# Kernel optimization log

Hardware: AMD Instinct MI355X
Metric: run time of the kernel (lower is better)

Reference implementation:

```python
import jax, jax.numpy as jnp
import numpy as np

B, T, D, H = 4096, 200, 128, 16
NEG = -4294967295.0  # -2**32 + 1, as in the TF source


def setup_inputs() -> dict:
    key = jax.random.key(0)
    k1, k2, k3, k4, k5 = jax.random.split(key, 5)
    query = jax.random.normal(k1, (B, D), dtype=jnp.float32)
    facts = jax.random.normal(k2, (B, T, D), dtype=jnp.float32)
    mask = jax.random.randint(k3, (B, T), 0, 2).astype(bool)
    mask = mask.at[:, 0].set(True)  # ensure at least one valid position per row
    W1 = jax.random.normal(k4, (4 * D, H), dtype=jnp.float32) * (1.0 / np.sqrt(4 * D))
    b1 = jnp.zeros((H,), dtype=jnp.float32)
    W2 = jax.random.normal(k5, (H, 1), dtype=jnp.float32) * (1.0 / np.sqrt(H))
    b2 = jnp.zeros((1,), dtype=jnp.float32)
    return {"query": query, "facts": facts, "mask": mask,
            "W1": W1, "b1": b1, "W2": W2, "b2": b2}


def reference(query, facts, mask, W1, b1, W2, b2):
    # query: [B, D], facts: [B, T, D], mask: [B, T] bool
    q = jnp.broadcast_to(query[:, None, :], facts.shape)          # [B, T, D]
    din_all = jnp.concatenate([q, facts, q - facts, q * facts], axis=-1)  # [B, T, 4D]
    h = jax.nn.sigmoid(jnp.einsum('btf,fh->bth', din_all, W1) + b1)       # [B, T, H]
    scores = (jnp.einsum('bth,ho->bto', h, W2) + b2)[..., 0]              # [B, T]
    scores = jnp.where(mask, scores, NEG)
    attn = jax.nn.softmax(scores, axis=-1)                                 # [B, T]
    out = jnp.einsum('bt,btd->bd', attn, facts)                            # [B, D]
    return out
```

## Files before the change

kernel.cpp:

```cpp
#include <hip/hip_runtime.h>

#define B_DIM 4096
#define T_DIM 200
#define D_DIM 128
#define H_DIM 16
#define NCH   25

typedef _Float16 h2 __attribute__((ext_vector_type(2)));
typedef __fp16   g2 __attribute__((ext_vector_type(2)));
union HU { unsigned int u; h2 h; };

__device__ __forceinline__ h2 pkh(float a, float b) {
    g2 t = __builtin_amdgcn_cvt_pkrtz(a, b);
    return __builtin_bit_cast(h2, t);
}

template<int CTRL>
__device__ __forceinline__ float dppmov(float x) {
    return __builtin_bit_cast(float,
        __builtin_amdgcn_update_dpp(0, __builtin_bit_cast(int, x), CTRL, 0xF, 0xF, true));
}
__device__ __forceinline__ float swz4f(float x) {
    return __builtin_bit_cast(float,
        __builtin_amdgcn_ds_swizzle(__builtin_bit_cast(int, x), 0x101F));
}

extern "C" __global__ __launch_bounds__(512)
void din_fused(const float* __restrict__ query,
               const float* __restrict__ facts,
               const int* __restrict__ mask,
               const float* __restrict__ W1,
               const float* __restrict__ b1,
               const float* __restrict__ W2,
               float* __restrict__ out)
{
    const int tid  = threadIdx.x;
    const int wid  = tid >> 6;
    const int lane = tid & 63;
    const int sub  = lane & 15;
    const int rg   = lane >> 4;
    const int b    = blockIdx.x * 8 + wid;

    __shared__ float W1bc[H_DIM * D_DIM];
    __shared__ float W1dd[H_DIM * D_DIM];
    __shared__ float W1ac[H_DIM * D_DIM];
    __shared__ unsigned int wef1[8][8 * 64];
    __shared__ float qwl[8][H_DIM];

    const float* fb = facts + (size_t)b * (T_DIM * D_DIM);
    const int*   mb = mask  + (size_t)b * T_DIM;
    const float* qb = query + (size_t)b * D_DIM;

    float4 FA[2][2], FB[2][2];
    int mvA[2], mvB[2];
    auto loadF = [&](int c, float4 (&F)[2][2], int (&mv)[2]) {
        int r0 = c * 8 + 2 * rg;
        #pragma unroll
        for (int k = 0; k < 2; ++k) {
            F[0][k] = *(const float4*)(fb + r0 * D_DIM     + sub * 8 + 4 * k);
            F[1][k] = *(const float4*)(fb + (r0+1) * D_DIM + sub * 8 + 4 * k);
        }
        mv[0] = mb[r0];
        mv[1] = mb[r0 + 1];
    };
    loadF(0, FA, mvA);

    #pragma unroll
    for (int i = 0; i < 4; ++i) {
        int idx = tid * 4 + i;
        int h = idx >> 7, d = idx & 127;
        W1bc[idx] = W1[(128 + d) * H_DIM + h] - W1[(256 + d) * H_DIM + h];
        W1dd[idx] = W1[(384 + d) * H_DIM + h];
        W1ac[idx] = W1[d * H_DIM + h] + W1[(256 + d) * H_DIM + h];
    }
    __syncthreads();

    {
        int h = lane & 15, dg = lane >> 4;
        float p = 0.f;
        #pragma unroll
        for (int k = 0; k < 8; ++k) {
            float4 a4 = *(const float4*)&W1ac[h * D_DIM + dg * 32 + 4 * k];
            float4 q4 = *(const float4*)(qb + dg * 32 + 4 * k);
            p += a4.x * q4.x + a4.y * q4.y + a4.z * q4.z + a4.w * q4.w;
        }
        p += __shfl_xor(p, 16);
        p += __shfl_xor(p, 32);
        if (lane < 16) qwl[wid][h] = p + b1[h];
    }
    {
        int h  = 8 + (lane >> 3);
        int p0 = (lane & 7) * 8;
        unsigned int pk[8];
        #pragma unroll
        for (int u = 0; u < 8; ++u) {
            int d0 = 2 * (p0 + u);
            float a0 = W1bc[h * D_DIM + d0]     + qb[d0]     * W1dd[h * D_DIM + d0];
            float a1 = W1bc[h * D_DIM + d0 + 1] + qb[d0 + 1] * W1dd[h * D_DIM + d0 + 1];
            HU t; t.h = pkh(a0, a1); pk[u] = t.u;
        }
        *(uint4*)&wef1[wid][(h - 8) * 64 + p0]     = make_uint4(pk[0], pk[1], pk[2], pk[3]);
        *(uint4*)&wef1[wid][(h - 8) * 64 + p0 + 4] = make_uint4(pk[4], pk[5], pk[6], pk[7]);
    }
    h2 wreg[8][4];
    {
        float qd[8];
        *(float4*)&qd[0] = *(const float4*)(qb + sub * 8);
        *(float4*)&qd[4] = *(const float4*)(qb + sub * 8 + 4);
        #pragma unroll
        for (int i = 0; i < 8; ++i) {
            #pragma unroll
            for (int j = 0; j < 4; ++j) {
                int d0 = sub * 8 + 2 * j;
                float a0 = W1bc[i * D_DIM + d0]     + qd[2*j]   * W1dd[i * D_DIM + d0];
                float a1 = W1bc[i * D_DIM + d0 + 1] + qd[2*j+1] * W1dd[i * D_DIM + d0 + 1];
                wreg[i][j] = pkh(a0, a1);
            }
        }
    }
    asm volatile("s_waitcnt lgkmcnt(0)" ::: "memory");

    const int hg = 4 * (sub & 1) + 2 * ((sub >> 1) & 1) + ((sub >> 3) & 1);
    const float qwA = qwl[wid][hg],     w2A = W2[hg];
    const float qwB = qwl[wid][hg + 8], w2B = W2[hg + 8];
    const unsigned int* wp = &wef1[wid][0];

    float a8[8];
    #pragma unroll
    for (int i = 0; i < 8; ++i) a8[i] = 0.f;
    float lloc = 0.f;

    auto process = [&](float4 (&F)[2][2], int (&mv)[2]) {
        h2 H[2][4];
        #pragma unroll
        for (int r = 0; r < 2; ++r) {
            H[r][0] = pkh(F[r][0].x, F[r][0].y);
            H[r][1] = pkh(F[r][0].z, F[r][0].w);
            H[r][2] = pkh(F[r][1].x, F[r][1].y);
            H[r][3] = pkh(F[r][1].z, F[r][1].w);
        }
        float sc0 = 0.f, sc1 = 0.f;
        #pragma unroll
        for (int g = 0; g < 2; ++g) {
            float hp0[8], hp1[8];
            #pragma unroll
            for (int i = 0; i < 8; ++i) {
                float t0 = 0.f, t1 = 0.f;
                if (g == 0) {
                    #pragma unroll
                    for (int j = 0; j < 4; ++j) {
                        t0 = __builtin_amdgcn_fdot2(wreg[i][j], H[0][j], t0, false);
                        t1 = __builtin_amdgcn_fdot2(wreg[i][j], H[1][j], t1, false);
                    }
                } else {
                    uint4 wl = *(const uint4*)&wp[i * 64 + sub * 4];
                    HU u0, u1, u2, u3;
                    u0.u = wl.x; u1.u = wl.y; u2.u = wl.z; u3.u = wl.w;
                    t0 = __builtin_amdgcn_fdot2(u0.h, H[0][0], t0, false);
                    t0 = __builtin_amdgcn_fdot2(u1.h, H[0][1], t0, false);
                    t0 = __builtin_amdgcn_fdot2(u2.h, H[0][2], t0, false);
                    t0 = __builtin_amdgcn_fdot2(u3.h, H[0][3], t0, false);
                    t1 = __builtin_amdgcn_fdot2(u0.h, H[1][0], t1, false);
                    t1 = __builtin_amdgcn_fdot2(u1.h, H[1][1], t1, false);
                    t1 = __builtin_amdgcn_fdot2(u2.h, H[1][2], t1, false);
                    t1 = __builtin_amdgcn_fdot2(u3.h, H[1][3], t1, false);
                }
                hp0[i] = t0; hp1[i] = t1;
            }
            #pragma unroll
            for (int i = 0; i < 4; ++i) {
                float k0 = (sub & 1) ? hp0[i + 4] : hp0[i];
                float s0 = (sub & 1) ? hp0[i]     : hp0[i + 4];
                hp0[i] = k0 + dppmov<0xB1>(s0);
                float k1 = (sub & 1) ? hp1[i + 4] : hp1[i];
                float s1 = (sub & 1) ? hp1[i]     : hp1[i + 4];
                hp1[i] = k1 + dppmov<0xB1>(s1);
            }
            #pragma unroll
            for (int i = 0; i < 2; ++i) {
                float k0 = (sub & 2) ? hp0[i + 2] : hp0[i];
                float s0 = (sub & 2) ? hp0[i]     : hp0[i + 2];
                hp0[i] = k0 + dppmov<0x4E>(s0);
                float k1 = (sub & 2) ? hp1[i + 2] : hp1[i];
                float s1 = (sub & 2) ? hp1[i]     : hp1[i + 2];
                hp1[i] = k1 + dppmov<0x4E>(s1);
            }
            {
                float k0 = (sub & 8) ? hp0[1] : hp0[0];
                float s0 = (sub & 8) ? hp0[0] : hp0[1];
                hp0[0] = k0 + dppmov<0x128>(s0);
                float k1 = (sub & 8) ? hp1[1] : hp1[0];
                float s1 = (sub & 8) ? hp1[0] : hp1[1];
                hp1[0] = k1 + dppmov<0x128>(s1);
            }
            hp0[0] += swz4f(hp0[0]);
            hp1[0] += swz4f(hp1[0]);
            float qs = g ? qwB : qwA, ws = g ? w2B : w2A;
            sc0 += ws / (1.f + __expf(-(qs + hp0[0])));
            sc1 += ws / (1.f + __expf(-(qs + hp1[0])));
        }
        sc0 += dppmov<0xB1>(sc0);
        sc0 += dppmov<0x4E>(sc0);
        sc0 += dppmov<0x128>(sc0);
        sc1 += dppmov<0xB1>(sc1);
        sc1 += dppmov<0x4E>(sc1);
        sc1 += dppmov<0x128>(sc1);
        float w0 = mv[0] ? __expf(sc0) : 0.f;
        float w1 = mv[1] ? __expf(sc1) : 0.f;
        lloc += w0 + w1;
        #pragma unroll
        for (int j = 0; j < 4; ++j) {
            a8[2*j]     += w0 * (float)H[0][j].x + w1 * (float)H[1][j].x;
            a8[2*j + 1] += w0 * (float)H[0][j].y + w1 * (float)H[1][j].y;
        }
    };

    #pragma unroll 1
    for (int c = 0; c < NCH - 1; c += 2) {
        loadF(c + 1, FB, mvB);
        process(FA, mvA);
        loadF(c + 2, FA, mvA);
        process(FB, mvB);
    }
    process(FA, mvA);

    float l = lloc;
    l += __shfl_xor(l, 16);
    l += __shfl_xor(l, 32);
    #pragma unroll
    for (int i = 0; i < 4; ++i) {
        float kp = (rg & 1) ? a8[i + 4] : a8[i];
        float sd = (rg & 1) ? a8[i]     : a8[i + 4];
        a8[i] = kp + __shfl_xor(sd, 16);
    }
    #pragma unroll
    for (int i = 0; i < 2; ++i) {
        float kp = (rg & 2) ? a8[i + 2] : a8[i];
        float sd = (rg & 2) ? a8[i]     : a8[i + 2];
        a8[i] = kp + __shfl_xor(sd, 32);
    }
    int dl = sub * 8 + 4 * (rg & 1) + 2 * ((rg >> 1) & 1);
    float inv = 1.f / l;
    *(float2*)(out + (size_t)b * D_DIM + dl) = make_float2(a8[0] * inv, a8[1] * inv);
}

extern "C" void kernel_launch(void* const* d_in, const int* in_sizes, int n_in,
                              void* d_out, int out_size, void* d_ws, size_t ws_size,
                              hipStream_t stream) {
    const float* query = (const float*)d_in[0];
    const float* facts = (const float*)d_in[1];
    const int*   mask  = (const int*)d_in[2];
    const float* W1    = (const float*)d_in[3];
    const float* b1    = (const float*)d_in[4];
    const float* W2    = (const float*)d_in[5];
    float* out = (float*)d_out;
    (void)in_sizes; (void)n_in; (void)out_size; (void)d_ws; (void)ws_size;

    din_fused<<<dim3(B_DIM / 8), dim3(512), 0, stream>>>(
        query, facts, mask, W1, b1, W2, out);
}
```

Baseline: 110.8 us.

## Move all packed W1 weights to LDS and triple-buffer facts prefetch

All 16 hidden units' query-folded fp16 weights now go into shared memory. Previously the first 8 were held in registers and only the second 8 in LDS. This frees about 32 VGPRs, which are spent on a third facts buffer so each wave keeps two chunks in flight instead of one, hiding more global-load latency in this bandwidth-bound loop. The cost is twice the LDS weight reads per chunk and a larger LDS footprint per block, which could lower occupancy or add LDS traffic.

```diff
diff --git a/kernel.cpp b/kernel.cpp
--- a/kernel.cpp
+++ b/kernel.cpp
@@ -44,15 +44,15 @@
     __shared__ float W1bc[H_DIM * D_DIM];
     __shared__ float W1dd[H_DIM * D_DIM];
     __shared__ float W1ac[H_DIM * D_DIM];
-    __shared__ unsigned int wef1[8][8 * 64];
+    __shared__ unsigned int wef[8][H_DIM * 64];
     __shared__ float qwl[8][H_DIM];
 
     const float* fb = facts + (size_t)b * (T_DIM * D_DIM);
     const int*   mb = mask  + (size_t)b * T_DIM;
     const float* qb = query + (size_t)b * D_DIM;
 
-    float4 FA[2][2], FB[2][2];
-    int mvA[2], mvB[2];
+    float4 FA[2][2], FB[2][2], FC[2][2];
+    int mvA[2], mvB[2], mvC[2];
     auto loadF = [&](int c, float4 (&F)[2][2], int (&mv)[2]) {
         int r0 = c * 8 + 2 * rg;
         #pragma unroll
@@ -64,6 +64,7 @@
         mv[1] = mb[r0 + 1];
     };
     loadF(0, FA, mvA);
+    loadF(1, FB, mvB);
 
     #pragma unroll
     for (int i = 0; i < 4; ++i) {
@@ -88,8 +89,9 @@
         p += __shfl_xor(p, 32);
         if (lane < 16) qwl[wid][h] = p + b1[h];
     }
-    {
-        int h  = 8 + (lane >> 3);
+    #pragma unroll
+    for (int pass = 0; pass < 2; ++pass) {
+        int h  = 8 * pass + (lane >> 3);
         int p0 = (lane & 7) * 8;
         unsigned int pk[8];
         #pragma unroll
@@ -99,31 +101,15 @@
             float a1 = W1bc[h * D_DIM + d0 + 1] + qb[d0 + 1] * W1dd[h * D_DIM + d0 + 1];
             HU t; t.h = pkh(a0, a1); pk[u] = t.u;
         }
-        *(uint4*)&wef1[wid][(h - 8) * 64 + p0]     = make_uint4(pk[0], pk[1], pk[2], pk[3]);
-        *(uint4*)&wef1[wid][(h - 8) * 64 + p0 + 4] = make_uint4(pk[4], pk[5], pk[6], pk[7]);
-    }
-    h2 wreg[8][4];
-    {
-        float qd[8];
-        *(float4*)&qd[0] = *(const float4*)(qb + sub * 8);
-        *(float4*)&qd[4] = *(const float4*)(qb + sub * 8 + 4);
-        #pragma unroll
-        for (int i = 0; i < 8; ++i) {
-            #pragma unroll
-            for (int j = 0; j < 4; ++j) {
-                int d0 = sub * 8 + 2 * j;
-                float a0 = W1bc[i * D_DIM + d0]     + qd[2*j]   * W1dd[i * D_DIM + d0];
-                float a1 = W1bc[i * D_DIM + d0 + 1] + qd[2*j+1] * W1dd[i * D_DIM + d0 + 1];
-                wreg[i][j] = pkh(a0, a1);
-            }
-        }
+        *(uint4*)&wef[wid][h * 64 + p0]     = make_uint4(pk[0], pk[1], pk[2], pk[3]);
+        *(uint4*)&wef[wid][h * 64 + p0 + 4] = make_uint4(pk[4], pk[5], pk[6], pk[7]);
     }
     asm volatile("s_waitcnt lgkmcnt(0)" ::: "memory");
 
     const int hg = 4 * (sub & 1) + 2 * ((sub >> 1) & 1) + ((sub >> 3) & 1);
     const float qwA = qwl[wid][hg],     w2A = W2[hg];
     const float qwB = qwl[wid][hg + 8], w2B = W2[hg + 8];
-    const unsigned int* wp = &wef1[wid][0];
+    const unsigned int* wp = &wef[wid][0];
 
     float a8[8];
     #pragma unroll
@@ -145,26 +131,18 @@
             float hp0[8], hp1[8];
             #pragma unroll
             for (int i = 0; i < 8; ++i) {
+                uint4 wl = *(const uint4*)&wp[(g * 8 + i) * 64 + sub * 4];
+                HU u0, u1, u2, u3;
+                u0.u = wl.x; u1.u = wl.y; u2.u = wl.z; u3.u = wl.w;
                 float t0 = 0.f, t1 = 0.f;
-                if (g == 0) {
-                    #pragma unroll
-                    for (int j = 0; j < 4; ++j) {
-                        t0 = __builtin_amdgcn_fdot2(wreg[i][j], H[0][j], t0, false);
-                        t1 = __builtin_amdgcn_fdot2(wreg[i][j], H[1][j], t1, false);
-                    }
-                } else {
-                    uint4 wl = *(const uint4*)&wp[i * 64 + sub * 4];
-                    HU u0, u1, u2, u3;
-                    u0.u = wl.x; u1.u = wl.y; u2.u = wl.z; u3.u = wl.w;
-                    t0 = __builtin_amdgcn_fdot2(u0.h, H[0][0], t0, false);
-                    t0 = __builtin_amdgcn_fdot2(u1.h, H[0][1], t0, false);
-                    t0 = __builtin_amdgcn_fdot2(u2.h, H[0][2], t0, false);
-                    t0 = __builtin_amdgcn_fdot2(u3.h, H[0][3], t0, false);
-                    t1 = __builtin_amdgcn_fdot2(u0.h, H[1][0], t1, false);
-                    t1 = __builtin_amdgcn_fdot2(u1.h, H[1][1], t1, false);
-                    t1 = __builtin_amdgcn_fdot2(u2.h, H[1][2], t1, false);
-                    t1 = __builtin_amdgcn_fdot2(u3.h, H[1][3], t1, false);
-                }
+                t0 = __builtin_amdgcn_fdot2(u0.h, H[0][0], t0, false);
+                t0 = __builtin_amdgcn_fdot2(u1.h, H[0][1], t0, false);
+                t0 = __builtin_amdgcn_fdot2(u2.h, H[0][2], t0, false);
+                t0 = __builtin_amdgcn_fdot2(u3.h, H[0][3], t0, false);
+                t1 = __builtin_amdgcn_fdot2(u0.h, H[1][0], t1, false);
+                t1 = __builtin_amdgcn_fdot2(u1.h, H[1][1], t1, false);
+                t1 = __builtin_amdgcn_fdot2(u2.h, H[1][2], t1, false);
+                t1 = __builtin_amdgcn_fdot2(u3.h, H[1][3], t1, false);
                 hp0[i] = t0; hp1[i] = t1;
             }
             #pragma unroll
@@ -216,11 +194,13 @@
     };
 
     #pragma unroll 1
-    for (int c = 0; c < NCH - 1; c += 2) {
-        loadF(c + 1, FB, mvB);
+    for (int c = 0; c < 24; c += 3) {
+        loadF(c + 2, FC, mvC);
         process(FA, mvA);
-        loadF(c + 2, FA, mvA);
+        loadF(c + 3, FA, mvA);
         process(FB, mvB);
+        if (c + 4 < NCH) loadF(c + 4, FB, mvB);
+        process(FC, mvC);
     }
     process(FA, mvA);
 
```

New measurement: 102.0 us. 1.09x faster.
